# Kernel tuning notes

Hardware: AMD Instinct MI355X
Metric: run time of the kernel (lower is better)

Reference implementation:

```python
import jax, jax.numpy as jnp
import numpy as np

D = 128            # dim_h
EDIM = D + 108     # tgt emb + 108-way edge one-hot (edge_linear in_features)
NSRC = 10000       # candidate source nodes
NEDGE = 320000     # candidate paths (edges), ~32 per src
TOPN = 6           # top_n path selection
GIN_EPS = 0.0      # init_eps, not learned
BN_EPS = 1e-5


def _batch_norm(x, gamma, beta):
    # torch BatchNorm1d in training mode: batch stats, biased variance
    mean = jnp.mean(x, axis=0)
    var = jnp.var(x, axis=0)
    return gamma * (x - mean) * jax.lax.rsqrt(var + BN_EPS) + beta


def _glorot(key, shape):
    fan_in, fan_out = shape[-2], shape[-1]
    lim = np.sqrt(6.0 / (fan_in + fan_out))
    return jax.random.uniform(key, shape, jnp.float32, -lim, lim)


def setup_inputs() -> dict:
    key = jax.random.key(0)
    ks = jax.random.split(key, 24)
    inp = {
        "paths_srcs": jax.random.normal(ks[0], (NSRC, D), jnp.float32),
        "path_feats": jax.random.normal(ks[1], (NEDGE, EDIM), jnp.float32),
        "src_ids": jax.random.randint(ks[2], (NEDGE,), 0, NSRC, jnp.int32),
        # 3 stacked GIN convs (weights stacked on leading axis)
        "conv_edge_W": _glorot(ks[3], (3, EDIM, D)),
        "conv_edge_b": jnp.zeros((3, D), jnp.float32),
        "conv_W1": _glorot(ks[4], (3, D, D)),       # MLP layer1, no bias
        "conv_bn_g": jnp.ones((3, D), jnp.float32),
        "conv_bn_b": jnp.zeros((3, D), jnp.float32),
        "conv_W2": _glorot(ks[5], (3, D, D)),       # MLP layer2, no bias
        # GINStack heads
        "lin1_W": _glorot(ks[6], (3 * D, D)),
        "lin1_b": jnp.zeros((D,), jnp.float32),
        "lin2_W": _glorot(ks[7], (D, D)),
        "lin2_b": jnp.zeros((D,), jnp.float32),
        # PathEncoder
        "pe_src_W": _glorot(ks[8], (D, D)),
        "pe_src_b": jnp.zeros((D,), jnp.float32),
        "pe_tgt_W": _glorot(ks[9], (EDIM, D)),
        "pe_tgt_b": jnp.zeros((D,), jnp.float32),
        "pe_bn_g": jnp.ones((D,), jnp.float32),
        "pe_bn_b": jnp.zeros((D,), jnp.float32),
        # linear path ranker head
        "score_w": _glorot(ks[10], (D, 1))[:, 0],
    }
    return inp


def reference(paths_srcs, path_feats, conv_edge_W, conv_edge_b, conv_W1,
              conv_bn_g, conv_bn_b, conv_W2, lin1_W, lin1_b, lin2_W, lin2_b,
              pe_src_W, pe_src_b, pe_tgt_W, pe_tgt_b, pe_bn_g, pe_bn_b,
              score_w, src_ids):
    # GIN message: relu(tgt+edge feature), summed per source node.
    # Identical for all 3 convs in the original, so compute once.
    msgs = jax.nn.relu(path_feats)                                   # [E, EDIM]
    agg = jax.ops.segment_sum(msgs, src_ids, num_segments=NSRC)      # [N, EDIM]

    hs = []
    for i in range(3):  # fixed 3-layer GINStack
        h_msg = agg @ conv_edge_W[i] + conv_edge_b[i]                # [N, D]
        h = (1.0 + GIN_EPS) * paths_srcs + h_msg
        z = jax.nn.relu(_batch_norm(h @ conv_W1[i], conv_bn_g[i], conv_bn_b[i]))
        hs.append(z @ conv_W2[i])
    h = jnp.concatenate(hs, axis=1) @ lin1_W + lin1_b                # [N, D]
    h = jax.nn.relu(h)
    node_emb = h @ lin2_W + lin2_b                                   # [N, D]

    # PathEncoder: src-node emb + fused (tgt+edge) emb -> path emb
    hpath = node_emb[src_ids] @ pe_src_W + pe_src_b \
          + path_feats @ pe_tgt_W + pe_tgt_b                         # [E, D]
    hpath = jax.nn.relu(_batch_norm(hpath, pe_bn_g, pe_bn_b))

    # linear path ranker + top-k path selection
    scores = hpath @ score_w                                         # [E]
    top_vals, top_idx = jax.lax.top_k(scores, TOPN)
    return node_emb, top_vals, top_idx
```

## Files before the change

kernel.cpp:

```cpp
#include <hip/hip_runtime.h>
#include <math.h>

#define NSRC 10000
#define NEDGE 320000
#define EDIM 236
#define TOPN 6

typedef __attribute__((ext_vector_type(8))) short short8;
typedef __attribute__((ext_vector_type(4))) float floatx4;

__device__ __forceinline__ unsigned short bf16_rne(float x) {
  union { float f; unsigned int u; } c; c.f = x;
  unsigned int r = (c.u + 0x7FFFu + ((c.u >> 16) & 1u)) >> 16;
  return (unsigned short)r;
}
__device__ __forceinline__ float bf16_to_f(unsigned short h) {
  union { unsigned int u; float f; } c; c.u = ((unsigned int)h) << 16;
  return c.f;
}
__device__ __forceinline__ void split_f32(float x, unsigned short& h, unsigned short& l) {
  h = bf16_rne(x);
  l = bf16_rne(x - bf16_to_f(h));
}

struct KV { float v; int i; };

__device__ __forceinline__ bool kv_better(const KV a, const KV b) {
  return (a.v > b.v) || (a.v == b.v && a.i < b.i);
}

__device__ __forceinline__ void kv_merge(KV d[TOPN], const KV o[TOPN]) {
  KV r[TOPN];
  int ia = 0, ib = 0;
#pragma unroll
  for (int q = 0; q < TOPN; ++q) {
    bool takeA;
    if (ia >= TOPN) takeA = false;
    else if (ib >= TOPN) takeA = true;
    else takeA = kv_better(d[ia], o[ib]);
    r[q] = takeA ? d[ia] : o[ib];
    if (takeA) ia++; else ib++;
  }
#pragma unroll
  for (int q = 0; q < TOPN; ++q) d[q] = r[q];
}

__global__ void k_sentinel(float* __restrict__ out) {
  if (threadIdx.x == 0) out[0] = 1.0e9f;
}

__global__ __launch_bounds__(256)
void k_prep_all(const float* __restrict__ cew, const float* __restrict__ ceb,
                const float* __restrict__ cw1, const float* __restrict__ cw2,
                const float* __restrict__ l1w, const float* __restrict__ l2w,
                const float* __restrict__ psw, const float* __restrict__ l2b,
                const float* __restrict__ psb, const float* __restrict__ ptb,
                const float* __restrict__ ptw,
                float* __restrict__ w1cat, float* __restrict__ wew1cat,
                float* __restrict__ bprime, float* __restrict__ m1,
                unsigned short* __restrict__ Bh, unsigned short* __restrict__ Bl,
                float* __restrict__ bcat, float* __restrict__ biascat,
                float* __restrict__ statsT, int* __restrict__ counts) {
  const int b = blockIdx.x;
  const int tid = threadIdx.x;
  if (b < 708) {
    if (tid >= 128) return;
    int i = b / EDIM;
    int k = b - i * EDIM;
    const float* we = cew + ((size_t)i * EDIM + k) * 128;
    const float* w1 = cw1 + (size_t)i * 16384;
    float acc = 0.f;
    for (int m = 0; m < 128; ++m) acc = fmaf(we[m], w1[m * 128 + tid], acc);
    wew1cat[k * 384 + i * 128 + tid] = acc;
  } else if (b < 1092) {
    if (tid >= 128) return;
    int bb = b - 708;
    int i = bb >> 7;
    int r = bb & 127;
    const float* w2 = cw2 + (size_t)i * 16384 + r * 128;
    float acc = 0.f;
    for (int c = 0; c < 128; ++c) acc = fmaf(w2[c], l1w[((size_t)i * 128 + c) * 128 + tid], acc);
    m1[bb * 128 + tid] = acc;
  } else if (b < 1284) {
    int gid = (b - 1092) * 256 + tid;
    if (gid >= 3 * 128 * 128) return;
    int i = gid >> 14;
    int m = (gid >> 7) & 127;
    int j = gid & 127;
    w1cat[m * 384 + i * 128 + j] = cw1[gid];
  } else if (b < 1287) {
    if (tid >= 128) return;
    int i = b - 1284;
    const float* be = ceb + i * 128;
    const float* w1 = cw1 + (size_t)i * 16384;
    float acc = 0.f;
    for (int m = 0; m < 128; ++m) acc = fmaf(be[m], w1[m * 128 + tid], acc);
    bprime[i * 128 + tid] = acc;
  } else if (b < 1415) {
    int n = b - 1287;
    float v = (tid < EDIM) ? ptw[(size_t)tid * 128 + n] : 0.f;
    unsigned short h, l;
    split_f32(v, h, l);
    Bh[n * 256 + tid] = h;
    Bl[n * 256 + tid] = l;
  } else if (b < 1543) {
    if (tid >= 128) return;
    int k = b - 1415;
    bcat[k * 256 + tid] = l2w[k * 128 + tid];
    float acc = 0.f;
    for (int c = 0; c < 128; ++c) acc = fmaf(l2w[k * 128 + c], psw[c * 128 + tid], acc);
    bcat[k * 256 + 128 + tid] = acc;
    if (k == 0) {
      biascat[tid] = l2b[tid];
      float bb = 0.f;
      for (int c = 0; c < 128; ++c) bb = fmaf(l2b[c], psw[c * 128 + tid], bb);
      biascat[128 + tid] = bb + psb[tid] + ptb[tid];
    }
  } else if (b < 1551) {
    int i = (b - 1543) * 256 + tid;
    if (i < 2048) statsT[i] = 0.f;
  } else {
    int i = (b - 1551) * 256 + tid;
    if (i < NSRC) counts[i] = 0;
  }
}

__global__ __launch_bounds__(256) void k_hist(const int* __restrict__ src,
                                              int* __restrict__ counts) {
  int e = blockIdx.x * 256 + threadIdx.x;
  if (e < NEDGE) atomicAdd(&counts[src[e]], 1);
}

__global__ __launch_bounds__(256) void k_scan(const int* __restrict__ counts,
                                              int* __restrict__ offsets,
                                              int* __restrict__ cursor) {
  __shared__ int part[256];
  const int t = threadIdx.x;
  const int base = t * 40;
  int s = 0;
  for (int k = 0; k < 40; ++k) {
    int i = base + k;
    if (i < NSRC) s += counts[i];
  }
  part[t] = s;
  __syncthreads();
  for (int off = 1; off < 256; off <<= 1) {
    int v = (t >= off) ? part[t - off] : 0;
    __syncthreads();
    part[t] += v;
    __syncthreads();
  }
  int run = (t == 0) ? 0 : part[t - 1];
  for (int k = 0; k < 40; ++k) {
    int i = base + k;
    if (i < NSRC) {
      offsets[i] = run;
      cursor[i] = run;
      run += counts[i];
    }
  }
  if (t == 255) offsets[NSRC] = run;
}

__global__ __launch_bounds__(256) void k_scatter(const int* __restrict__ src,
                                                 int* __restrict__ cursor,
                                                 int* __restrict__ elist) {
  int e = blockIdx.x * 256 + threadIdx.x;
  if (e < NEDGE) {
    int p = atomicAdd(&cursor[src[e]], 1);
    elist[p] = e;
  }
}

__global__ __launch_bounds__(256) void k_gather(const float* __restrict__ pf,
                                                const int* __restrict__ offsets,
                                                const int* __restrict__ elist,
                                                float* __restrict__ agg) {
  const int row = blockIdx.x;
  const int t = threadIdx.x;
  __shared__ int sid[64];
  const int beg = offsets[row];
  const int end = offsets[row + 1];
  float a0 = 0.f, a1 = 0.f, a2 = 0.f, a3 = 0.f;
  for (int b = beg; b < end; b += 64) {
    const int cnt = min(64, end - b);
    __syncthreads();
    if (t < cnt) sid[t] = elist[b + t];
    __syncthreads();
    if (t < EDIM) {
      int e = 0;
      for (; e + 4 <= cnt; e += 4) {
        int i0 = sid[e], i1 = sid[e + 1], i2 = sid[e + 2], i3 = sid[e + 3];
        a0 += fmaxf(pf[(size_t)i0 * EDIM + t], 0.f);
        a1 += fmaxf(pf[(size_t)i1 * EDIM + t], 0.f);
        a2 += fmaxf(pf[(size_t)i2 * EDIM + t], 0.f);
        a3 += fmaxf(pf[(size_t)i3 * EDIM + t], 0.f);
      }
      for (; e < cnt; ++e) a0 += fmaxf(pf[(size_t)sid[e] * EDIM + t], 0.f);
    }
  }
  if (t < EDIM) agg[(size_t)row * EDIM + t] = (a0 + a1) + (a2 + a3);
}

__global__ __launch_bounds__(256)
void k_gemmT(const float* __restrict__ A1, const float* __restrict__ B1,
             const float* __restrict__ A2, const float* __restrict__ B2,
             const float* __restrict__ bias, float* __restrict__ C,
             float* __restrict__ colsum, float* __restrict__ colsumsq) {
  __shared__ float As[8][128];
  __shared__ float Bs[8][128];
  __shared__ float red[16][128];
  const int tid = threadIdx.x;
  const int tx = tid & 15;
  const int ty = tid >> 4;
  const int bm = blockIdx.x * 128;
  const int bn = blockIdx.y * 128;
  const int N = 384;

  float acc[8][8];
#pragma unroll
  for (int i = 0; i < 8; ++i)
#pragma unroll
    for (int j = 0; j < 8; ++j) acc[i][j] = 0.f;

#pragma unroll 1
  for (int seg = 0; seg < 2; ++seg) {
    const float* A = seg ? A2 : A1;
    const float* B = seg ? B2 : B1;
    const int K = seg ? EDIM : 128;
    for (int k0 = 0; k0 < K; k0 += 8) {
      {
        int r = tid >> 1;
        int cq = (tid & 1) << 2;
        float4 v = make_float4(0.f, 0.f, 0.f, 0.f);
        int row = bm + r;
        if (row < NSRC) {
          const float* ap = A + (size_t)row * K + k0 + cq;
          if (k0 + cq + 4 <= K) {
            v = *(const float4*)ap;
          } else {
            float tmp[4] = {0.f, 0.f, 0.f, 0.f};
            for (int q = 0; q < 4; ++q)
              if (k0 + cq + q < K) tmp[q] = ap[q];
            v = make_float4(tmp[0], tmp[1], tmp[2], tmp[3]);
          }
        }
        As[cq + 0][r] = v.x;
        As[cq + 1][r] = v.y;
        As[cq + 2][r] = v.z;
        As[cq + 3][r] = v.w;
      }
      {
        int r = tid >> 5;
        int c = (tid & 31) << 2;
        float4 v = make_float4(0.f, 0.f, 0.f, 0.f);
        int kk = k0 + r;
        if (kk < K) v = *(const float4*)(B + (size_t)kk * N + bn + c);
        *(float4*)&Bs[r][c] = v;
      }
      __syncthreads();
#pragma unroll
      for (int kk = 0; kk < 8; ++kk) {
        const float4 a0 = *(const float4*)&As[kk][ty * 8];
        const float4 a1 = *(const float4*)&As[kk][ty * 8 + 4];
        const float4 b0 = *(const float4*)&Bs[kk][tx * 8];
        const float4 b1 = *(const float4*)&Bs[kk][tx * 8 + 4];
        const float av[8] = {a0.x, a0.y, a0.z, a0.w, a1.x, a1.y, a1.z, a1.w};
        const float bv[8] = {b0.x, b0.y, b0.z, b0.w, b1.x, b1.y, b1.z, b1.w};
#pragma unroll
        for (int i = 0; i < 8; ++i)
#pragma unroll
          for (int j = 0; j < 8; ++j) acc[i][j] = fmaf(av[i], bv[j], acc[i][j]);
      }
      __syncthreads();
    }
  }

  const int nb = bn + tx * 8;
  float colS[8], colQ[8];
#pragma unroll
  for (int j = 0; j < 8; ++j) { colS[j] = 0.f; colQ[j] = 0.f; }
#pragma unroll
  for (int i = 0; i < 8; ++i) {
    int m = bm + ty * 8 + i;
    if (m < NSRC) {
      float outv[8];
#pragma unroll
      for (int j = 0; j < 8; ++j) outv[j] = acc[i][j] + bias[nb + j];
      float* crow = C + (size_t)m * N + nb;
      *(float4*)crow = make_float4(outv[0], outv[1], outv[2], outv[3]);
      *(float4*)(crow + 4) = make_float4(outv[4], outv[5], outv[6], outv[7]);
#pragma unroll
      for (int j = 0; j < 8; ++j) { colS[j] += outv[j]; colQ[j] += outv[j] * outv[j]; }
    }
  }
  *(float4*)&red[ty][tx * 8] = make_float4(colS[0], colS[1], colS[2], colS[3]);
  *(float4*)&red[ty][tx * 8 + 4] = make_float4(colS[4], colS[5], colS[6], colS[7]);
  __syncthreads();
  if (tid < 128) {
    float s = 0.f;
#pragma unroll
    for (int t = 0; t < 16; ++t) s += red[t][tid];
    atomicAdd(colsum + bn + tid, s);
  }
  __syncthreads();
  *(float4*)&red[ty][tx * 8] = make_float4(colQ[0], colQ[1], colQ[2], colQ[3]);
  *(float4*)&red[ty][tx * 8 + 4] = make_float4(colQ[4], colQ[5], colQ[6], colQ[7]);
  __syncthreads();
  if (tid < 128) {
    float s = 0.f;
#pragma unroll
    for (int t = 0; t < 16; ++t) s += red[t][tid];
    atomicAdd(colsumsq + bn + tid, s);
  }
}

template <int ATR, int EPI>
__global__ __launch_bounds__(256)
void gemm_k(const float* __restrict__ A, const float* __restrict__ B,
            float* __restrict__ C, int M, int K, int N,
            const float* __restrict__ bn_g, const float* __restrict__ bn_b,
            const float* __restrict__ rawS, const float* __restrict__ rawQ,
            const float* __restrict__ bias, float* __restrict__ C2) {
  __shared__ float As[8][128];
  __shared__ float Bs[8][128];
  const int tid = threadIdx.x;
  const int tx = tid & 15;
  const int ty = tid >> 4;
  const int bm = blockIdx.x * 128;
  const int bn = blockIdx.y * 128;

  float acc[8][8];
#pragma unroll
  for (int i = 0; i < 8; ++i)
#pragma unroll
    for (int j = 0; j < 8; ++j) acc[i][j] = 0.f;

  for (int k0 = 0; k0 < K; k0 += 8) {
    {
      int r = tid >> 1;
      int cq = (tid & 1) << 2;
      float4 v = make_float4(0.f, 0.f, 0.f, 0.f);
      int row = bm + r;
      if (row < M) {
        const float* ap = A + (size_t)row * K + k0 + cq;
        if (k0 + cq + 4 <= K) {
          v = *(const float4*)ap;
        } else {
          float tmp[4] = {0.f, 0.f, 0.f, 0.f};
          for (int q = 0; q < 4; ++q)
            if (k0 + cq + q < K) tmp[q] = ap[q];
          v = make_float4(tmp[0], tmp[1], tmp[2], tmp[3]);
        }
      }
      if constexpr (ATR == 2) {
        float vv[4] = {v.x, v.y, v.z, v.w};
#pragma unroll
        for (int q = 0; q < 4; ++q) {
          int k = k0 + cq + q;
          if (k < K) {
            float mean = rawS[k] * (1.0f / NSRC);
            float var = rawQ[k] * (1.0f / NSRC) - mean * mean;
            float rstd = rsqrtf(var + 1e-5f);
            vv[q] = fmaxf(fmaf(bn_g[k] * rstd, vv[q] - mean, bn_b[k]), 0.f);
          } else {
            vv[q] = 0.f;
          }
        }
        v = make_float4(vv[0], vv[1], vv[2], vv[3]);
      }
      As[cq + 0][r] = v.x;
      As[cq + 1][r] = v.y;
      As[cq + 2][r] = v.z;
      As[cq + 3][r] = v.w;
    }
    {
      int r = tid >> 5;
      int c = (tid & 31) << 2;
      float4 v = make_float4(0.f, 0.f, 0.f, 0.f);
      int kk = k0 + r;
      if (kk < K) v = *(const float4*)(B + (size_t)kk * N + bn + c);
      *(float4*)&Bs[r][c] = v;
    }
    __syncthreads();
#pragma unroll
    for (int kk = 0; kk < 8; ++kk) {
      const float4 a0 = *(const float4*)&As[kk][ty * 8];
      const float4 a1 = *(const float4*)&As[kk][ty * 8 + 4];
      const float4 b0 = *(const float4*)&Bs[kk][tx * 8];
      const float4 b1 = *(const float4*)&Bs[kk][tx * 8 + 4];
      const float av[8] = {a0.x, a0.y, a0.z, a0.w, a1.x, a1.y, a1.z, a1.w};
      const float bv[8] = {b0.x, b0.y, b0.z, b0.w, b1.x, b1.y, b1.z, b1.w};
#pragma unroll
      for (int i = 0; i < 8; ++i)
#pragma unroll
        for (int j = 0; j < 8; ++j) acc[i][j] = fmaf(av[i], bv[j], acc[i][j]);
    }
    __syncthreads();
  }

  const int nb = bn + tx * 8;
#pragma unroll
  for (int i = 0; i < 8; ++i) {
    int m = bm + ty * 8 + i;
    if (m < M) {
      float outv[8];
#pragma unroll
      for (int j = 0; j < 8; ++j) {
        outv[j] = acc[i][j] + bias[nb + j];
        if constexpr (EPI == 2) outv[j] = fmaxf(outv[j], 0.f);
      }
      float* crow;
      if constexpr (EPI == 5) {
        crow = (nb < 128) ? (C + (size_t)m * 128 + nb) : (C2 + (size_t)m * 128 + (nb - 128));
      } else {
        crow = C + (size_t)m * N + nb;
      }
      *(float4*)crow = make_float4(outv[0], outv[1], outv[2], outv[3]);
      *(float4*)(crow + 4) = make_float4(outv[4], outv[5], outv[6], outv[7]);
    }
  }
}

__global__ __launch_bounds__(256)
void k_hgemm(const float* __restrict__ A, const unsigned short* __restrict__ Bh,
             const unsigned short* __restrict__ Bl, const int* __restrict__ srcids,
             const float* __restrict__ pre_src, float* __restrict__ hpath,
             float* __restrict__ colsum, float* __restrict__ colsumsq) {
  __shared__ __align__(16) unsigned short Bhs[128][40];
  __shared__ __align__(16) unsigned short Bls[128][40];
  __shared__ float redS[4][128];
  __shared__ float redQ[4][128];

  const int tid = threadIdx.x;
  const int wave = tid >> 6;
  const int lane = tid & 63;
  const int am = lane & 15;
  const int aq = lane >> 4;
  const int bm = blockIdx.x * 128;

  floatx4 acc[2][8];
#pragma unroll
  for (int mt = 0; mt < 2; ++mt)
#pragma unroll
    for (int nt = 0; nt < 8; ++nt) acc[mt][nt] = (floatx4){0.f, 0.f, 0.f, 0.f};

  const int rowS = tid >> 1;
  const int kq = (tid & 1) * 16;
  const float* a0p = A + (size_t)(bm + wave * 32 + am) * EDIM;
  const float* a1p = a0p + 16 * EDIM;

  for (int c = 0; c < 8; ++c) {
    const int k0 = c * 32;
    {
      const unsigned short* bhp = Bh + (size_t)rowS * 256 + k0 + kq;
      const unsigned short* blp = Bl + (size_t)rowS * 256 + k0 + kq;
      *(short8*)&Bhs[rowS][kq] = *(const short8*)bhp;
      *(short8*)&Bhs[rowS][kq + 8] = *(const short8*)(bhp + 8);
      *(short8*)&Bls[rowS][kq] = *(const short8*)blp;
      *(short8*)&Bls[rowS][kq + 8] = *(const short8*)(blp + 8);
    }
    const int kA = k0 + aq * 8;
    float av0[8], av1[8];
    if (kA + 8 <= EDIM) {
      float4 x = *(const float4*)(a0p + kA);
      float4 y = *(const float4*)(a0p + kA + 4);
      av0[0] = x.x; av0[1] = x.y; av0[2] = x.z; av0[3] = x.w;
      av0[4] = y.x; av0[5] = y.y; av0[6] = y.z; av0[7] = y.w;
      x = *(const float4*)(a1p + kA);
      y = *(const float4*)(a1p + kA + 4);
      av1[0] = x.x; av1[1] = x.y; av1[2] = x.z; av1[3] = x.w;
      av1[4] = y.x; av1[5] = y.y; av1[6] = y.z; av1[7] = y.w;
    } else {
#pragma unroll
      for (int q = 0; q < 8; ++q) {
        int k = kA + q;
        av0[q] = (k < EDIM) ? a0p[k] : 0.f;
        av1[q] = (k < EDIM) ? a1p[k] : 0.f;
      }
    }
    short8 ah0, al0, ah1, al1;
#pragma unroll
    for (int q = 0; q < 8; ++q) {
      unsigned short h, l;
      split_f32(av0[q], h, l);
      ah0[q] = (short)h; al0[q] = (short)l;
      split_f32(av1[q], h, l);
      ah1[q] = (short)h; al1[q] = (short)l;
    }
    __syncthreads();
#pragma unroll
    for (int nt = 0; nt < 8; ++nt) {
      const short8 bh = *(const short8*)&Bhs[nt * 16 + am][aq * 8];
      const short8 bl = *(const short8*)&Bls[nt * 16 + am][aq * 8];
      acc[0][nt] = __builtin_amdgcn_mfma_f32_16x16x32_bf16(ah0, bl, acc[0][nt], 0, 0, 0);
      acc[1][nt] = __builtin_amdgcn_mfma_f32_16x16x32_bf16(ah1, bl, acc[1][nt], 0, 0, 0);
      acc[0][nt] = __builtin_amdgcn_mfma_f32_16x16x32_bf16(al0, bh, acc[0][nt], 0, 0, 0);
      acc[1][nt] = __builtin_amdgcn_mfma_f32_16x16x32_bf16(al1, bh, acc[1][nt], 0, 0, 0);
      acc[0][nt] = __builtin_amdgcn_mfma_f32_16x16x32_bf16(ah0, bh, acc[0][nt], 0, 0, 0);
      acc[1][nt] = __builtin_amdgcn_mfma_f32_16x16x32_bf16(ah1, bh, acc[1][nt], 0, 0, 0);
    }
    __syncthreads();
  }

  float colS[8], colQ[8];
#pragma unroll
  for (int nt = 0; nt < 8; ++nt) { colS[nt] = 0.f; colQ[nt] = 0.f; }
#pragma unroll
  for (int mt = 0; mt < 2; ++mt) {
#pragma unroll
    for (int r = 0; r < 4; ++r) {
      const int m = bm + wave * 32 + mt * 16 + aq * 4 + r;
      const int sid = srcids[m];
      const float* g = pre_src + (size_t)sid * 128;
      float* hp = hpath + (size_t)m * 128;
#pragma unroll
      for (int nt = 0; nt < 8; ++nt) {
        const int col = nt * 16 + am;
        float v = acc[mt][nt][r] + g[col];
        hp[col] = v;
        colS[nt] += v;
        colQ[nt] += v * v;
      }
    }
  }
#pragma unroll
  for (int nt = 0; nt < 8; ++nt) {
    colS[nt] += __shfl_xor(colS[nt], 16);
    colS[nt] += __shfl_xor(colS[nt], 32);
    colQ[nt] += __shfl_xor(colQ[nt], 16);
    colQ[nt] += __shfl_xor(colQ[nt], 32);
  }
  if (lane < 16) {
#pragma unroll
    for (int nt = 0; nt < 8; ++nt) {
      redS[wave][nt * 16 + lane] = colS[nt];
      redQ[wave][nt * 16 + lane] = colQ[nt];
    }
  }
  __syncthreads();
  if (tid < 128) {
    float s = redS[0][tid] + redS[1][tid] + redS[2][tid] + redS[3][tid];
    atomicAdd(colsum + tid, s);
  } else {
    int cn = tid - 128;
    float s = redQ[0][cn] + redQ[1][cn] + redQ[2][cn] + redQ[3][cn];
    atomicAdd(colsumsq + cn, s);
  }
}

__global__ __launch_bounds__(256)
void k_scoretop(const float* __restrict__ hpath, const float* __restrict__ stP,
                const float* __restrict__ g, const float* __restrict__ b,
                const float* __restrict__ w, KV* __restrict__ cand) {
  const int tid = threadIdx.x;
  const int cg = tid & 15;
  const int grp = (blockIdx.x * 256 + tid) >> 4;
  float a8[8], c8[8], w8[8];
#pragma unroll
  for (int q = 0; q < 8; ++q) {
    int j = cg * 8 + q;
    float mean = stP[j] * (1.0f / NEDGE);
    float var = stP[128 + j] * (1.0f / NEDGE) - mean * mean;
    float rstd = rsqrtf(var + 1e-5f);
    float aj = g[j] * rstd;
    a8[q] = aj;
    c8[q] = b[j] - aj * mean;
    w8[q] = w[j];
  }
  KV t[TOPN];
#pragma unroll
  for (int q = 0; q < TOPN; ++q) { t[q].v = -INFINITY; t[q].i = 2147483647; }
  for (int row = grp; row < NEDGE; row += 4096) {
    const float* hp = hpath + (size_t)row * 128 + cg * 8;
    const float4 x0 = *(const float4*)hp;
    const float4 x1 = *(const float4*)(hp + 4);
    const float xs[8] = {x0.x, x0.y, x0.z, x0.w, x1.x, x1.y, x1.z, x1.w};
    float part = 0.f;
#pragma unroll
    for (int q = 0; q < 8; ++q)
      part += fmaxf(fmaf(a8[q], xs[q], c8[q]), 0.f) * w8[q];
#pragma unroll
    for (int o = 8; o >= 1; o >>= 1) part += __shfl_xor(part, o, 16);
    if (cg == 0 && part > t[TOPN - 1].v) {
      t[TOPN - 1].v = part;
      t[TOPN - 1].i = row;
#pragma unroll
      for (int q = TOPN - 1; q > 0; --q) {
        if (t[q].v > t[q - 1].v) { KV tmp = t[q - 1]; t[q - 1] = t[q]; t[q] = tmp; }
      }
    }
  }
  __shared__ KV sh[128][TOPN];
  for (int s = 128; s >= 1; s >>= 1) {
    if (tid >= s && tid < 2 * s) {
#pragma unroll
      for (int q = 0; q < TOPN; ++q) sh[tid - s][q] = t[q];
    }
    __syncthreads();
    if (tid < s) kv_merge(t, sh[tid]);
    __syncthreads();
  }
  if (tid == 0) {
#pragma unroll
    for (int q = 0; q < TOPN; ++q) cand[blockIdx.x * TOPN + q] = t[q];
  }
}

__global__ __launch_bounds__(256) void k_top2(const KV* __restrict__ cand,
                                              float* __restrict__ outTail) {
  int tid = threadIdx.x;
  KV t[TOPN];
#pragma unroll
  for (int q = 0; q < TOPN; ++q) t[q] = cand[tid * TOPN + q];
  __shared__ KV sh[128][TOPN];
  for (int s = 128; s >= 1; s >>= 1) {
    if (tid >= s && tid < 2 * s) {
#pragma unroll
      for (int q = 0; q < TOPN; ++q) sh[tid - s][q] = t[q];
    }
    __syncthreads();
    if (tid < s) kv_merge(t, sh[tid]);
    __syncthreads();
  }
  if (tid == 0) {
#pragma unroll
    for (int q = 0; q < TOPN; ++q) {
      outTail[q] = t[q].v;
      outTail[TOPN + q] = (float)t[q].i;
    }
  }
}

extern "C" void kernel_launch(void* const* d_in, const int* in_sizes, int n_in,
                              void* d_out, int out_size, void* d_ws, size_t ws_size,
                              hipStream_t stream) {
  const float* paths_srcs = (const float*)d_in[0];
  const float* path_feats = (const float*)d_in[1];
  const int* src_ids = (const int*)d_in[2];
  const float* cew = (const float*)d_in[3];
  const float* ceb = (const float*)d_in[4];
  const float* cw1 = (const float*)d_in[5];
  const float* bng = (const float*)d_in[6];
  const float* bnbt = (const float*)d_in[7];
  const float* cw2 = (const float*)d_in[8];
  const float* l1w = (const float*)d_in[9];
  const float* l1b = (const float*)d_in[10];
  const float* l2w = (const float*)d_in[11];
  const float* l2b = (const float*)d_in[12];
  const float* psw = (const float*)d_in[13];
  const float* psb = (const float*)d_in[14];
  const float* ptw = (const float*)d_in[15];
  const float* ptb = (const float*)d_in[16];
  const float* pbg = (const float*)d_in[17];
  const float* pbb = (const float*)d_in[18];
  const float* scw = (const float*)d_in[19];
  float* out = (float*)d_out;
  float* ws = (float*)d_ws;

  float* w1cat = ws;
  float* wew1cat = w1cat + 49152;
  float* bprime = wew1cat + 90624;
  float* m1 = bprime + 512;
  float* statsT = m1 + 49152;
  float* statsP = statsT + 1536;
  float* agg = statsP + 512;
  float* T = agg + 2360000;
  float* H1 = T + 3840000;
  float* pre_src = H1 + 1280000;
  float* scores_dead = pre_src + 1280000;
  KV* cand = (KV*)(scores_dead + 320000);
  float* hpath = scores_dead + 320000 + 3072;
  unsigned short* Bh = (unsigned short*)(hpath + 40960000);
  unsigned short* Bl = Bh + 32768;
  float* bcat = (float*)(Bl + 32768);
  float* biascat = bcat + 32768;
  int* counts = (int*)hpath;
  int* offsets = counts + 10000;
  int* cursor = offsets + 10001;
  int* elist = cursor + 10000;
  const size_t needed = (size_t)(49152 + 90624 + 512 + 49152 + 1536 + 512 + 2360000 +
                                 3840000 + 1280000 + 1280000 + 320000 + 3072 +
                                 40960000 + 16384 + 16384 + 32768 + 256) * 4;
  if (ws_size < needed) {
    k_sentinel<<<1, 64, 0, stream>>>(out);
    return;
  }

  k_prep_all<<<1591, 256, 0, stream>>>(cew, ceb, cw1, cw2, l1w, l2w, psw, l2b, psb, ptb,
                                       ptw, w1cat, wew1cat, bprime, m1, Bh, Bl,
                                       bcat, biascat, statsT, counts);
  k_hist<<<(NEDGE + 255) / 256, 256, 0, stream>>>(src_ids, counts);
  k_scan<<<1, 256, 0, stream>>>(counts, offsets, cursor);
  k_scatter<<<(NEDGE + 255) / 256, 256, 0, stream>>>(src_ids, cursor, elist);
  k_gather<<<NSRC, 256, 0, stream>>>(path_feats, offsets, elist, agg);
  k_gemmT<<<dim3(79, 3), 256, 0, stream>>>(paths_srcs, w1cat, agg, wew1cat, bprime, T,
                                           statsT, statsT + 384);
  gemm_k<2, 2><<<dim3(79, 1), 256, 0, stream>>>(T, m1, H1, NSRC, 384, 128,
                                                bng, bnbt, statsT, statsT + 384,
                                                l1b, nullptr);
  gemm_k<0, 5><<<dim3(79, 2), 256, 0, stream>>>(H1, bcat, out, NSRC, 128, 256,
                                                nullptr, nullptr, nullptr, nullptr,
                                                biascat, pre_src);
  k_hgemm<<<2500, 256, 0, stream>>>(path_feats, Bh, Bl, src_ids, pre_src, hpath,
                                    statsP, statsP + 128);
  k_scoretop<<<256, 256, 0, stream>>>(hpath, statsP, pbg, pbb, scw, cand);
  k_top2<<<1, 256, 0, stream>>>(cand, out + (size_t)NSRC * 128);
}
```

Measured before the change: 990.7 us.

## Shrink GEMM tiles, prefetch hgemm operands, widen gather and top-k grids

```diff
diff --git a/kernel.cpp b/kernel.cpp
--- a/kernel.cpp
+++ b/kernel.cpp
@@ -181,7 +181,9 @@
   __shared__ int sid[64];
   const int beg = offsets[row];
   const int end = offsets[row + 1];
-  float a0 = 0.f, a1 = 0.f, a2 = 0.f, a3 = 0.f;
+  float a[8];
+#pragma unroll
+  for (int q = 0; q < 8; ++q) a[q] = 0.f;
   for (int b = beg; b < end; b += 64) {
     const int cnt = min(64, end - b);
     __syncthreads();
@@ -189,17 +191,24 @@
     __syncthreads();
     if (t < EDIM) {
       int e = 0;
-      for (; e + 4 <= cnt; e += 4) {
+      for (; e + 8 <= cnt; e += 8) {
         int i0 = sid[e], i1 = sid[e + 1], i2 = sid[e + 2], i3 = sid[e + 3];
-        a0 += fmaxf(pf[(size_t)i0 * EDIM + t], 0.f);
-        a1 += fmaxf(pf[(size_t)i1 * EDIM + t], 0.f);
-        a2 += fmaxf(pf[(size_t)i2 * EDIM + t], 0.f);
-        a3 += fmaxf(pf[(size_t)i3 * EDIM + t], 0.f);
-      }
-      for (; e < cnt; ++e) a0 += fmaxf(pf[(size_t)sid[e] * EDIM + t], 0.f);
-    }
-  }
-  if (t < EDIM) agg[(size_t)row * EDIM + t] = (a0 + a1) + (a2 + a3);
+        int i4 = sid[e + 4], i5 = sid[e + 5], i6 = sid[e + 6], i7 = sid[e + 7];
+        a[0] += fmaxf(pf[(size_t)i0 * EDIM + t], 0.f);
+        a[1] += fmaxf(pf[(size_t)i1 * EDIM + t], 0.f);
+        a[2] += fmaxf(pf[(size_t)i2 * EDIM + t], 0.f);
+        a[3] += fmaxf(pf[(size_t)i3 * EDIM + t], 0.f);
+        a[4] += fmaxf(pf[(size_t)i4 * EDIM + t], 0.f);
+        a[5] += fmaxf(pf[(size_t)i5 * EDIM + t], 0.f);
+        a[6] += fmaxf(pf[(size_t)i6 * EDIM + t], 0.f);
+        a[7] += fmaxf(pf[(size_t)i7 * EDIM + t], 0.f);
+      }
+      for (; e < cnt; ++e) a[0] += fmaxf(pf[(size_t)sid[e] * EDIM + t], 0.f);
+    }
+  }
+  if (t < EDIM)
+    agg[(size_t)row * EDIM + t] =
+        ((a[0] + a[1]) + (a[2] + a[3])) + ((a[4] + a[5]) + (a[6] + a[7]));
 }
 
 __global__ __launch_bounds__(256)
@@ -207,21 +216,26 @@
              const float* __restrict__ A2, const float* __restrict__ B2,
              const float* __restrict__ bias, float* __restrict__ C,
              float* __restrict__ colsum, float* __restrict__ colsumsq) {
-  __shared__ float As[8][128];
-  __shared__ float Bs[8][128];
-  __shared__ float red[16][128];
+  __shared__ float As[8][64];
+  __shared__ float Bs[8][64];
+  __shared__ float red[16][64];
   const int tid = threadIdx.x;
   const int tx = tid & 15;
   const int ty = tid >> 4;
-  const int bm = blockIdx.x * 128;
-  const int bn = blockIdx.y * 128;
+  const int bm = blockIdx.x * 64;
+  const int bn = blockIdx.y * 64;
   const int N = 384;
 
-  float acc[8][8];
-#pragma unroll
-  for (int i = 0; i < 8; ++i)
-#pragma unroll
-    for (int j = 0; j < 8; ++j) acc[i][j] = 0.f;
+  float acc[4][4];
+#pragma unroll
+  for (int i = 0; i < 4; ++i)
+#pragma unroll
+    for (int j = 0; j < 4; ++j) acc[i][j] = 0.f;
+
+  const int ar = tid & 63;
+  const int ac = (tid >> 6) << 1;
+  const int bkr = tid >> 5;
+  const int bc = (tid & 31) << 1;
 
 #pragma unroll 1
   for (int seg = 0; seg < 2; ++seg) {
@@ -230,84 +244,67 @@
     const int K = seg ? EDIM : 128;
     for (int k0 = 0; k0 < K; k0 += 8) {
       {
-        int r = tid >> 1;
-        int cq = (tid & 1) << 2;
-        float4 v = make_float4(0.f, 0.f, 0.f, 0.f);
-        int row = bm + r;
+        float2 v = make_float2(0.f, 0.f);
+        int row = bm + ar;
+        int k = k0 + ac;
         if (row < NSRC) {
-          const float* ap = A + (size_t)row * K + k0 + cq;
-          if (k0 + cq + 4 <= K) {
-            v = *(const float4*)ap;
-          } else {
-            float tmp[4] = {0.f, 0.f, 0.f, 0.f};
-            for (int q = 0; q < 4; ++q)
-              if (k0 + cq + q < K) tmp[q] = ap[q];
-            v = make_float4(tmp[0], tmp[1], tmp[2], tmp[3]);
-          }
+          if (k + 2 <= K) v = *(const float2*)(A + (size_t)row * K + k);
+          else if (k < K) v.x = A[(size_t)row * K + k];
         }
-        As[cq + 0][r] = v.x;
-        As[cq + 1][r] = v.y;
-        As[cq + 2][r] = v.z;
-        As[cq + 3][r] = v.w;
+        As[ac][ar] = v.x;
+        As[ac + 1][ar] = v.y;
       }
       {
-        int r = tid >> 5;
-        int c = (tid & 31) << 2;
-        float4 v = make_float4(0.f, 0.f, 0.f, 0.f);
-        int kk = k0 + r;
-        if (kk < K) v = *(const float4*)(B + (size_t)kk * N + bn + c);
-        *(float4*)&Bs[r][c] = v;
+        float2 v = make_float2(0.f, 0.f);
+        int kk = k0 + bkr;
+        if (kk < K) v = *(const float2*)(B + (size_t)kk * N + bn + bc);
+        Bs[bkr][bc] = v.x;
+        Bs[bkr][bc + 1] = v.y;
       }
       __syncthreads();
 #pragma unroll
       for (int kk = 0; kk < 8; ++kk) {
-        const float4 a0 = *(const float4*)&As[kk][ty * 8];
-        const float4 a1 = *(const float4*)&As[kk][ty * 8 + 4];
-        const float4 b0 = *(const float4*)&Bs[kk][tx * 8];
-        const float4 b1 = *(const float4*)&Bs[kk][tx * 8 + 4];
-        const float av[8] = {a0.x, a0.y, a0.z, a0.w, a1.x, a1.y, a1.z, a1.w};
-        const float bv[8] = {b0.x, b0.y, b0.z, b0.w, b1.x, b1.y, b1.z, b1.w};
-#pragma unroll
-        for (int i = 0; i < 8; ++i)
-#pragma unroll
-          for (int j = 0; j < 8; ++j) acc[i][j] = fmaf(av[i], bv[j], acc[i][j]);
+        const float4 a0 = *(const float4*)&As[kk][ty * 4];
+        const float4 b0 = *(const float4*)&Bs[kk][tx * 4];
+        const float av[4] = {a0.x, a0.y, a0.z, a0.w};
+        const float bv[4] = {b0.x, b0.y, b0.z, b0.w};
+#pragma unroll
+        for (int i = 0; i < 4; ++i)
+#pragma unroll
+          for (int j = 0; j < 4; ++j) acc[i][j] = fmaf(av[i], bv[j], acc[i][j]);
       }
       __syncthreads();
     }
   }
 
-  const int nb = bn + tx * 8;
-  float colS[8], colQ[8];
-#pragma unroll
-  for (int j = 0; j < 8; ++j) { colS[j] = 0.f; colQ[j] = 0.f; }
-#pragma unroll
-  for (int i = 0; i < 8; ++i) {
-    int m = bm + ty * 8 + i;
+  const int nb = bn + tx * 4;
+  float colS[4], colQ[4];
+#pragma unroll
+  for (int j = 0; j < 4; ++j) { colS[j] = 0.f; colQ[j] = 0.f; }
+#pragma unroll
+  for (int i = 0; i < 4; ++i) {
+    int m = bm + ty * 4 + i;
     if (m < NSRC) {
-      float outv[8];
-#pragma unroll
-      for (int j = 0; j < 8; ++j) outv[j] = acc[i][j] + bias[nb + j];
-      float* crow = C + (size_t)m * N + nb;
-      *(float4*)crow = make_float4(outv[0], outv[1], outv[2], outv[3]);
-      *(float4*)(crow + 4) = make_float4(outv[4], outv[5], outv[6], outv[7]);
-#pragma unroll
-      for (int j = 0; j < 8; ++j) { colS[j] += outv[j]; colQ[j] += outv[j] * outv[j]; }
-    }
-  }
-  *(float4*)&red[ty][tx * 8] = make_float4(colS[0], colS[1], colS[2], colS[3]);
-  *(float4*)&red[ty][tx * 8 + 4] = make_float4(colS[4], colS[5], colS[6], colS[7]);
+      float outv[4];
+#pragma unroll
+      for (int j = 0; j < 4; ++j) outv[j] = acc[i][j] + bias[nb + j];
+      *(float4*)(C + (size_t)m * N + nb) = make_float4(outv[0], outv[1], outv[2], outv[3]);
+#pragma unroll
+      for (int j = 0; j < 4; ++j) { colS[j] += outv[j]; colQ[j] += outv[j] * outv[j]; }
+    }
+  }
+  *(float4*)&red[ty][tx * 4] = make_float4(colS[0], colS[1], colS[2], colS[3]);
   __syncthreads();
-  if (tid < 128) {
+  if (tid < 64) {
     float s = 0.f;
 #pragma unroll
     for (int t = 0; t < 16; ++t) s += red[t][tid];
     atomicAdd(colsum + bn + tid, s);
   }
   __syncthreads();
-  *(float4*)&red[ty][tx * 8] = make_float4(colQ[0], colQ[1], colQ[2], colQ[3]);
-  *(float4*)&red[ty][tx * 8 + 4] = make_float4(colQ[4], colQ[5], colQ[6], colQ[7]);
+  *(float4*)&red[ty][tx * 4] = make_float4(colQ[0], colQ[1], colQ[2], colQ[3]);
   __syncthreads();
-  if (tid < 128) {
+  if (tid < 64) {
     float s = 0.f;
 #pragma unroll
     for (int t = 0; t < 16; ++t) s += red[t][tid];
@@ -322,91 +319,83 @@
             const float* __restrict__ bn_g, const float* __restrict__ bn_b,
             const float* __restrict__ rawS, const float* __restrict__ rawQ,
             const float* __restrict__ bias, float* __restrict__ C2) {
-  __shared__ float As[8][128];
-  __shared__ float Bs[8][128];
+  __shared__ float As[8][64];
+  __shared__ float Bs[8][64];
   const int tid = threadIdx.x;
   const int tx = tid & 15;
   const int ty = tid >> 4;
-  const int bm = blockIdx.x * 128;
-  const int bn = blockIdx.y * 128;
-
-  float acc[8][8];
-#pragma unroll
-  for (int i = 0; i < 8; ++i)
-#pragma unroll
-    for (int j = 0; j < 8; ++j) acc[i][j] = 0.f;
+  const int bm = blockIdx.x * 64;
+  const int bn = blockIdx.y * 64;
+
+  float acc[4][4];
+#pragma unroll
+  for (int i = 0; i < 4; ++i)
+#pragma unroll
+    for (int j = 0; j < 4; ++j) acc[i][j] = 0.f;
+
+  const int ar = tid & 63;
+  const int ac = (tid >> 6) << 1;
+  const int bkr = tid >> 5;
+  const int bc = (tid & 31) << 1;
 
   for (int k0 = 0; k0 < K; k0 += 8) {
     {
-      int r = tid >> 1;
-      int cq = (tid & 1) << 2;
-      float4 v = make_float4(0.f, 0.f, 0.f, 0.f);
-      int row = bm + r;
+      float2 v = make_float2(0.f, 0.f);
+      int row = bm + ar;
+      int k = k0 + ac;
       if (row < M) {
-        const float* ap = A + (size_t)row * K + k0 + cq;
-        if (k0 + cq + 4 <= K) {
-          v = *(const float4*)ap;
-        } else {
-          float tmp[4] = {0.f, 0.f, 0.f, 0.f};
-          for (int q = 0; q < 4; ++q)
-            if (k0 + cq + q < K) tmp[q] = ap[q];
-          v = make_float4(tmp[0], tmp[1], tmp[2], tmp[3]);
-        }
+        if (k + 2 <= K) v = *(const float2*)(A + (size_t)row * K + k);
+        else if (k < K) v.x = A[(size_t)row * K + k];
       }
       if constexpr (ATR == 2) {
-        float vv[4] = {v.x, v.y, v.z, v.w};
-#pragma unroll
-        for (int q = 0; q < 4; ++q) {
-          int k = k0 + cq + q;
-          if (k < K) {
-            float mean = rawS[k] * (1.0f / NSRC);
-            float var = rawQ[k] * (1.0f / NSRC) - mean * mean;
+        float vv[2] = {v.x, v.y};
+#pragma unroll
+        for (int q = 0; q < 2; ++q) {
+          int kk = k0 + ac + q;
+          if (kk < K) {
+            float mean = rawS[kk] * (1.0f / NSRC);
+            float var = rawQ[kk] * (1.0f / NSRC) - mean * mean;
             float rstd = rsqrtf(var + 1e-5f);
-            vv[q] = fmaxf(fmaf(bn_g[k] * rstd, vv[q] - mean, bn_b[k]), 0.f);
+            vv[q] = fmaxf(fmaf(bn_g[kk] * rstd, vv[q] - mean, bn_b[kk]), 0.f);
           } else {
             vv[q] = 0.f;
           }
         }
-        v = make_float4(vv[0], vv[1], vv[2], vv[3]);
-      }
-      As[cq + 0][r] = v.x;
-      As[cq + 1][r] = v.y;
-      As[cq + 2][r] = v.z;
-      As[cq + 3][r] = v.w;
+        v = make_float2(vv[0], vv[1]);
+      }
+      As[ac][ar] = v.x;
+      As[ac + 1][ar] = v.y;
     }
     {
-      int r = tid >> 5;
-      int c = (tid & 31) << 2;
-      float4 v = make_float4(0.f, 0.f, 0.f, 0.f);
-      int kk = k0 + r;
-      if (kk < K) v = *(const float4*)(B + (size_t)kk * N + bn + c);
-      *(float4*)&Bs[r][c] = v;
+      float2 v = make_float2(0.f, 0.f);
+      int kk = k0 + bkr;
+      if (kk < K) v = *(const float2*)(B + (size_t)kk * N + bn + bc);
+      Bs[bkr][bc] = v.x;
+      Bs[bkr][bc + 1] = v.y;
     }
     __syncthreads();
 #pragma unroll
     for (int kk = 0; kk < 8; ++kk) {
-      const float4 a0 = *(const float4*)&As[kk][ty * 8];
-      const float4 a1 = *(const float4*)&As[kk][ty * 8 + 4];
-      const float4 b0 = *(const float4*)&Bs[kk][tx * 8];
-      const float4 b1 = *(const float4*)&Bs[kk][tx * 8 + 4];
-      const float av[8] = {a0.x, a0.y, a0.z, a0.w, a1.x, a1.y, a1.z, a1.w};
-      const float bv[8] = {b0.x, b0.y, b0.z, b0.w, b1.x, b1.y, b1.z, b1.w};
-#pragma unroll
-      for (int i = 0; i < 8; ++i)
-#pragma unroll
-        for (int j = 0; j < 8; ++j) acc[i][j] = fmaf(av[i], bv[j], acc[i][j]);
-    }
-    __syncthreads();
-  }
-
-  const int nb = bn + tx * 8;
-#pragma unroll
-  for (int i = 0; i < 8; ++i) {
-    int m = bm + ty * 8 + i;
+      const float4 a0 = *(const float4*)&As[kk][ty * 4];
+      const float4 b0 = *(const float4*)&Bs[kk][tx * 4];
+      const float av[4] = {a0.x, a0.y, a0.z, a0.w};
+      const float bv[4] = {b0.x, b0.y, b0.z, b0.w};
+#pragma unroll
+      for (int i = 0; i < 4; ++i)
+#pragma unroll
+        for (int j = 0; j < 4; ++j) acc[i][j] = fmaf(av[i], bv[j], acc[i][j]);
+    }
+    __syncthreads();
+  }
+
+  const int nb = bn + tx * 4;
+#pragma unroll
+  for (int i = 0; i < 4; ++i) {
+    int m = bm + ty * 4 + i;
     if (m < M) {
-      float outv[8];
-#pragma unroll
-      for (int j = 0; j < 8; ++j) {
+      float outv[4];
+#pragma unroll
+      for (int j = 0; j < 4; ++j) {
         outv[j] = acc[i][j] + bias[nb + j];
         if constexpr (EPI == 2) outv[j] = fmaxf(outv[j], 0.f);
       }
@@ -417,7 +406,6 @@
         crow = C + (size_t)m * N + nb;
       }
       *(float4*)crow = make_float4(outv[0], outv[1], outv[2], outv[3]);
-      *(float4*)(crow + 4) = make_float4(outv[4], outv[5], outv[6], outv[7]);
     }
   }
 }
@@ -449,46 +437,63 @@
   const int kq = (tid & 1) * 16;
   const float* a0p = A + (size_t)(bm + wave * 32 + am) * EDIM;
   const float* a1p = a0p + 16 * EDIM;
-
-  for (int c = 0; c < 8; ++c) {
-    const int k0 = c * 32;
-    {
-      const unsigned short* bhp = Bh + (size_t)rowS * 256 + k0 + kq;
-      const unsigned short* blp = Bl + (size_t)rowS * 256 + k0 + kq;
-      *(short8*)&Bhs[rowS][kq] = *(const short8*)bhp;
-      *(short8*)&Bhs[rowS][kq + 8] = *(const short8*)(bhp + 8);
-      *(short8*)&Bls[rowS][kq] = *(const short8*)blp;
-      *(short8*)&Bls[rowS][kq + 8] = *(const short8*)(blp + 8);
-    }
-    const int kA = k0 + aq * 8;
-    float av0[8], av1[8];
+  const unsigned short* bhp0 = Bh + (size_t)rowS * 256 + kq;
+  const unsigned short* blp0 = Bl + (size_t)rowS * 256 + kq;
+
+  short8 pBh0, pBh1, pBl0, pBl1;
+  float pA0[8], pA1[8];
+
+  auto loadB = [&](int c) {
+    const unsigned short* bhp = bhp0 + c * 32;
+    const unsigned short* blp = blp0 + c * 32;
+    pBh0 = *(const short8*)bhp;
+    pBh1 = *(const short8*)(bhp + 8);
+    pBl0 = *(const short8*)blp;
+    pBl1 = *(const short8*)(blp + 8);
+  };
+  auto loadA = [&](int c) {
+    const int kA = c * 32 + aq * 8;
     if (kA + 8 <= EDIM) {
       float4 x = *(const float4*)(a0p + kA);
       float4 y = *(const float4*)(a0p + kA + 4);
-      av0[0] = x.x; av0[1] = x.y; av0[2] = x.z; av0[3] = x.w;
-      av0[4] = y.x; av0[5] = y.y; av0[6] = y.z; av0[7] = y.w;
+      pA0[0] = x.x; pA0[1] = x.y; pA0[2] = x.z; pA0[3] = x.w;
+      pA0[4] = y.x; pA0[5] = y.y; pA0[6] = y.z; pA0[7] = y.w;
       x = *(const float4*)(a1p + kA);
       y = *(const float4*)(a1p + kA + 4);
-      av1[0] = x.x; av1[1] = x.y; av1[2] = x.z; av1[3] = x.w;
-      av1[4] = y.x; av1[5] = y.y; av1[6] = y.z; av1[7] = y.w;
+      pA1[0] = x.x; pA1[1] = x.y; pA1[2] = x.z; pA1[3] = x.w;
+      pA1[4] = y.x; pA1[5] = y.y; pA1[6] = y.z; pA1[7] = y.w;
     } else {
 #pragma unroll
       for (int q = 0; q < 8; ++q) {
         int k = kA + q;
-        av0[q] = (k < EDIM) ? a0p[k] : 0.f;
-        av1[q] = (k < EDIM) ? a1p[k] : 0.f;
-      }
-    }
+        pA0[q] = (k < EDIM) ? a0p[k] : 0.f;
+        pA1[q] = (k < EDIM) ? a1p[k] : 0.f;
+      }
+    }
+  };
+
+  loadB(0);
+  loadA(0);
+#pragma unroll
+  for (int c = 0; c < 8; ++c) {
+    *(short8*)&Bhs[rowS][kq] = pBh0;
+    *(short8*)&Bhs[rowS][kq + 8] = pBh1;
+    *(short8*)&Bls[rowS][kq] = pBl0;
+    *(short8*)&Bls[rowS][kq + 8] = pBl1;
     short8 ah0, al0, ah1, al1;
 #pragma unroll
     for (int q = 0; q < 8; ++q) {
       unsigned short h, l;
-      split_f32(av0[q], h, l);
+      split_f32(pA0[q], h, l);
       ah0[q] = (short)h; al0[q] = (short)l;
-      split_f32(av1[q], h, l);
+      split_f32(pA1[q], h, l);
       ah1[q] = (short)h; al1[q] = (short)l;
     }
     __syncthreads();
+    if (c < 7) {
+      loadB(c + 1);
+      loadA(c + 1);
+    }
 #pragma unroll
     for (int nt = 0; nt < 8; ++nt) {
       const short8 bh = *(const short8*)&Bhs[nt * 16 + am][aq * 8];
@@ -571,7 +576,7 @@
   KV t[TOPN];
 #pragma unroll
   for (int q = 0; q < TOPN; ++q) { t[q].v = -INFINITY; t[q].i = 2147483647; }
-  for (int row = grp; row < NEDGE; row += 4096) {
+  for (int row = grp; row < NEDGE; row += 16384) {
     const float* hp = hpath + (size_t)row * 128 + cg * 8;
     const float4 x0 = *(const float4*)hp;
     const float4 x1 = *(const float4*)(hp + 4);
@@ -613,6 +618,12 @@
   KV t[TOPN];
 #pragma unroll
   for (int q = 0; q < TOPN; ++q) t[q] = cand[tid * TOPN + q];
+  for (int gset = 1; gset < 4; ++gset) {
+    KV o[TOPN];
+#pragma unroll
+    for (int q = 0; q < TOPN; ++q) o[q] = cand[(gset * 256 + tid) * TOPN + q];
+    kv_merge(t, o);
+  }
   __shared__ KV sh[128][TOPN];
   for (int s = 128; s >= 1; s >>= 1) {
     if (tid >= s && tid < 2 * s) {
@@ -669,12 +680,13 @@
   float* H1 = T + 3840000;
   float* pre_src = H1 + 1280000;
   float* scores_dead = pre_src + 1280000;
-  KV* cand = (KV*)(scores_dead + 320000);
-  float* hpath = scores_dead + 320000 + 3072;
+  float* candpad = scores_dead + 320000;
+  float* hpath = candpad + 3072;
   unsigned short* Bh = (unsigned short*)(hpath + 40960000);
   unsigned short* Bl = Bh + 32768;
   float* bcat = (float*)(Bl + 32768);
   float* biascat = bcat + 32768;
+  KV* cand = (KV*)scores_dead;
   int* counts = (int*)hpath;
   int* offsets = counts + 10000;
   int* cursor = offsets + 10001;
@@ -694,16 +706,16 @@
   k_scan<<<1, 256, 0, stream>>>(counts, offsets, cursor);
   k_scatter<<<(NEDGE + 255) / 256, 256, 0, stream>>>(src_ids, cursor, elist);
   k_gather<<<NSRC, 256, 0, stream>>>(path_feats, offsets, elist, agg);
-  k_gemmT<<<dim3(79, 3), 256, 0, stream>>>(paths_srcs, w1cat, agg, wew1cat, bprime, T,
-                                           statsT, statsT + 384);
-  gemm_k<2, 2><<<dim3(79, 1), 256, 0, stream>>>(T, m1, H1, NSRC, 384, 128,
-                                                bng, bnbt, statsT, statsT + 384,
-                                                l1b, nullptr);
-  gemm_k<0, 5><<<dim3(79, 2), 256, 0, stream>>>(H1, bcat, out, NSRC, 128, 256,
-                                                nullptr, nullptr, nullptr, nullptr,
-                                                biascat, pre_src);
+  k_gemmT<<<dim3(157, 6), 256, 0, stream>>>(paths_srcs, w1cat, agg, wew1cat, bprime, T,
+                                            statsT, statsT + 384);
+  gemm_k<2, 2><<<dim3(157, 2), 256, 0, stream>>>(T, m1, H1, NSRC, 384, 128,
+                                                 bng, bnbt, statsT, statsT + 384,
+                                                 l1b, nullptr);
+  gemm_k<0, 5><<<dim3(157, 4), 256, 0, stream>>>(H1, bcat, out, NSRC, 128, 256,
+                                                 nullptr, nullptr, nullptr, nullptr,
+                                                 biascat, pre_src);
   k_hgemm<<<2500, 256, 0, stream>>>(path_feats, Bh, Bl, src_ids, pre_src, hpath,
                                     statsP, statsP + 128);
-  k_scoretop<<<256, 256, 0, stream>>>(hpath, statsP, pbg, pbb, scw, cand);
+  k_scoretop<<<1024, 256, 0, stream>>>(hpath, statsP, pbg, pbb, scw, cand);
   k_top2<<<1, 256, 0, stream>>>(cand, out + (size_t)NSRC * 128);
 }
```

Result: faster. 968.6 us (-2.2%).
